# Kernel tuning notes

Measured on AMD Instinct MI355X. Metric: run time of the kernel, lower is better.

The kernel has to match this reference:

```python
import jax, jax.numpy as jnp
import numpy as np

BN_EPS = 1e-5


def setup_inputs() -> dict:
    key = jax.random.key(0)
    ks = jax.random.split(key, 12)
    N, E, H, INV = 100000, 500000, 128, 16
    DIN = 2 * H + INV  # 272
    x_send = jax.random.normal(ks[0], (N, H), dtype=jnp.float32)
    x_rec = jax.random.normal(ks[1], (N, H), dtype=jnp.float32)
    index = jax.random.randint(ks[2], (2, E), 0, N, dtype=jnp.int64)
    edge_attr = jax.random.normal(ks[3], (E, INV), dtype=jnp.float32)
    # message_mlp = BatchNorm1d(272) -> Linear(272,128) -> SiLU  (eval-mode BN)
    bn_gamma = jax.random.normal(ks[4], (DIN,), dtype=jnp.float32) * 0.1 + 1.0
    bn_beta = jax.random.normal(ks[5], (DIN,), dtype=jnp.float32) * 0.1
    bn_mean = jax.random.normal(ks[6], (DIN,), dtype=jnp.float32) * 0.1
    bn_var = jax.random.uniform(ks[7], (DIN,), dtype=jnp.float32) + 0.5
    W1 = jax.random.normal(ks[8], (DIN, H), dtype=jnp.float32) / np.sqrt(DIN)
    b1 = jnp.zeros((H,), dtype=jnp.float32)
    # edge_inf_mlp = Linear(128,1) -> Sigmoid
    W2 = jax.random.normal(ks[9], (H, 1), dtype=jnp.float32) / np.sqrt(H)
    b2 = jnp.zeros((1,), dtype=jnp.float32)
    return {"x_send": x_send, "x_rec": x_rec, "index": index, "edge_attr": edge_attr,
            "bn_gamma": bn_gamma, "bn_beta": bn_beta, "bn_mean": bn_mean, "bn_var": bn_var,
            "W1": W1, "b1": b1, "W2": W2, "b2": b2}


def reference(x_send, x_rec, index, edge_attr, bn_gamma, bn_beta, bn_mean, bn_var, W1, b1, W2, b2):
    idx_send, idx_rec = index[0], index[1]
    # gather + concat -> [E, 2H + INV]
    state = jnp.concatenate((x_send[idx_send], x_rec[idx_rec], edge_attr), axis=1)
    # eval-mode BatchNorm1d
    state = (state - bn_mean) * (bn_gamma * jax.lax.rsqrt(bn_var + BN_EPS)) + bn_beta
    # Linear + SiLU
    messages = jax.nn.silu(state @ W1 + b1)  # [E, H]
    # edge gating: Linear(H,1) + Sigmoid
    edge_weights = jax.nn.sigmoid(messages @ W2 + b2)  # [E, 1]
    # scatter_add aggregation over receiving nodes
    return jax.ops.segment_sum(messages * edge_weights, idx_rec, num_segments=x_rec.shape[0])
```

## Files before the change

kernel.cpp:

```cpp
#include <hip/hip_runtime.h>
#include <hip/hip_bf16.h>
#include <hip/hip_fp16.h>
#include <math.h>

#define HDIM 128
#define INVD 16
#define DIN 272
#define NKT 9

typedef __attribute__((ext_vector_type(4))) float f32x4;
typedef __attribute__((ext_vector_type(8))) short bf16x8;
typedef __attribute__((ext_vector_type(2))) __fp16 fp16x2;

__device__ inline short f2bf(float f) {
    union { float f; unsigned u; } v; v.f = f;
    unsigned r = v.u + 0x7FFFu + ((v.u >> 16) & 1u);
    return (short)(r >> 16);
}

__device__ inline unsigned cvt_pk_bf16(float a, float b) {
    unsigned r;
    asm("v_cvt_pk_bf16_f32 %0, %1, %2" : "=v"(r) : "v"(a), "v"(b));
    return r;
}

template<int MODE>
__global__ __launch_bounds__(256, 2) void etnn_kernel(
    const float* __restrict__ x_send,
    const float* __restrict__ x_rec,
    const int*   __restrict__ index,
    const float* __restrict__ edge_attr,
    const float* __restrict__ bn_gamma,
    const float* __restrict__ bn_beta,
    const float* __restrict__ bn_mean,
    const float* __restrict__ bn_var,
    const float* __restrict__ W1,
    const float* __restrict__ b1,
    const float* __restrict__ W2,
    const float* __restrict__ b2,
    float* __restrict__ out,
    __half* __restrict__ ws,
    int E, int nIter)
{
    __shared__ short btab[NKT * 8 * 64 * 8];
    __shared__ float scl[DIN];
    __shared__ float shf[DIN];
    __shared__ float bias2[2][HDIM];
    __shared__ float biasT[HDIM];

    const int tid = threadIdx.x;
    const int l  = tid & 63;
    const int lr = l & 15;
    const int lg = l >> 4;

    for (int c = tid; c < DIN; c += 256) {
        float sc = bn_gamma[c] * rsqrtf(bn_var[c] + 1e-5f);
        scl[c] = sc;
        shf[c] = bn_beta[c] - bn_mean[c] * sc;
    }
    __syncthreads();

    for (int f = tid; f < NKT * 8 * 64; f += 256) {
        const int kk  = f >> 9;
        const int cb  = (f >> 6) & 7;
        const int ln  = f & 63;
        const int k0  = kk * 32 + (ln >> 4) * 8;
        const int col = cb * 16 + (ln & 15);
        bf16x8 bv;
        #pragma unroll
        for (int j = 0; j < 8; ++j) {
            const int k = k0 + j;
            float v = (k < DIN) ? scl[k] * W1[k * HDIM + col] : 0.f;
            bv[j] = f2bf(v);
        }
        *(bf16x8*)&btab[f * 8] = bv;
    }
    {
        const int col  = tid & 127;
        const int half = tid >> 7;
        float s = 0.f;
        for (int k = half * 136; k < half * 136 + 136; ++k)
            s += shf[k] * W1[k * HDIM + col];
        bias2[half][col] = s;
    }
    __syncthreads();
    if (tid < HDIM) biasT[tid] = b1[tid] + bias2[0][tid] + bias2[1][tid];
    __syncthreads();

    float biasv[8], w2v[8];
    #pragma unroll
    for (int cb = 0; cb < 8; ++cb) {
        biasv[cb] = biasT[cb * 16 + lr];
        w2v[cb]   = W2[cb * 16 + lr];
    }
    const float b2v = b2[0];
    const bool evn = !(lr & 1);

    auto issueGather = [&](int pc, int is, int ir,
                           f32x4* Ls, f32x4* Lr, f32x4* La) {
        const f32x4* ps = (const f32x4*)(x_send + (size_t)is * HDIM);
        const f32x4* pr = (const f32x4*)(x_rec  + (size_t)ir * HDIM);
        #pragma unroll
        for (int kk = 0; kk < 4; ++kk) {
            Ls[kk * 2]     = ps[kk * 8 + lg * 2];
            Ls[kk * 2 + 1] = ps[kk * 8 + lg * 2 + 1];
            Lr[kk * 2]     = pr[kk * 8 + lg * 2];
            Lr[kk * 2 + 1] = pr[kk * 8 + lg * 2 + 1];
        }
        if (lg < 2) {
            const f32x4* pa = (const f32x4*)(edge_attr + (size_t)pc * INVD + lg * 8);
            La[0] = pa[0]; La[1] = pa[1];
        } else {
            La[0] = (f32x4){0.f, 0.f, 0.f, 0.f};
            La[1] = (f32x4){0.f, 0.f, 0.f, 0.f};
        }
    };

    auto computeTile = [&](int e0, int ir,
                           f32x4* Ls, f32x4* Lr, f32x4* La) {
        f32x4 acc[8];
        #pragma unroll
        for (int cb = 0; cb < 8; ++cb) acc[cb] = (f32x4){0.f, 0.f, 0.f, 0.f};

        #pragma unroll
        for (int kk = 0; kk < NKT; ++kk) {
            f32x4 lo = (kk < 4) ? Ls[kk * 2]     : (kk < 8) ? Lr[(kk - 4) * 2]     : La[0];
            f32x4 hi = (kk < 4) ? Ls[kk * 2 + 1] : (kk < 8) ? Lr[(kk - 4) * 2 + 1] : La[1];
            union { bf16x8 v; unsigned u[4]; } a;
            a.u[0] = cvt_pk_bf16(lo[0], lo[1]);
            a.u[1] = cvt_pk_bf16(lo[2], lo[3]);
            a.u[2] = cvt_pk_bf16(hi[0], hi[1]);
            a.u[3] = cvt_pk_bf16(hi[2], hi[3]);
            #pragma unroll
            for (int cb = 0; cb < 8; ++cb) {
                bf16x8 b = *(const bf16x8*)&btab[((kk * 8 + cb) * 64 + l) * 8];
                acc[cb] = __builtin_amdgcn_mfma_f32_16x16x32_bf16(a.v, b, acc[cb], 0, 0, 0);
            }
        }

        float p[4] = {0.f, 0.f, 0.f, 0.f};
        #pragma unroll
        for (int cb = 0; cb < 8; ++cb) {
            #pragma unroll
            for (int q = 0; q < 4; ++q) {
                float z = acc[cb][q] + biasv[cb];
                float m = z / (1.f + __expf(-z));
                acc[cb][q] = m;
                p[q] += m * w2v[cb];
            }
        }
        #pragma unroll
        for (int q = 0; q < 4; ++q) {
            p[q] += __shfl_xor(p[q], 1, 64);
            p[q] += __shfl_xor(p[q], 2, 64);
            p[q] += __shfl_xor(p[q], 4, 64);
            p[q] += __shfl_xor(p[q], 8, 64);
        }

        #pragma unroll
        for (int q = 0; q < 4; ++q) {
            const int row = lg * 4 + q;
            if (e0 + row < E) {
                const int irq = __shfl(ir, row, 64);
                const float g = 1.f / (1.f + __expf(-(p[q] + b2v)));
                if constexpr (MODE == 1) {
                    float m[8];
                    #pragma unroll
                    for (int cb = 0; cb < 8; ++cb) m[cb] = acc[cb][q] * g;
                    #pragma unroll
                    for (int c = 0; c < 4; ++c) {
                        float x0 = __shfl_xor(m[2 * c],     1, 64);
                        float x1 = __shfl_xor(m[2 * c + 1], 1, 64);
                        float va = evn ? m[2 * c] : x1;
                        float vb = evn ? x0       : m[2 * c + 1];
                        union { fp16x2 h; unsigned u; } pk;
                        pk.h = __builtin_amdgcn_cvt_pkrtz(va, vb);
                        const int col0 = evn ? (32 * c + lr) : (32 * c + 15 + lr);
                        unsigned long long a =
                            (unsigned long long)(ws + (size_t)irq * HDIM + col0);
                        asm volatile("global_atomic_pk_add_f16 %0, %1, off"
                                     :: "v"(a), "v"(pk.u) : "memory");
                    }
                } else {
                    float* orow = out + (size_t)irq * HDIM + lr;
                    #pragma unroll
                    for (int cb = 0; cb < 8; ++cb)
                        atomicAdd(orow + cb * 16, acc[cb][q] * g);
                }
            }
        }
    };

    const int gw = blockIdx.x * 4 + (tid >> 6);
    const int NW = gridDim.x * 4;

    for (int it = gw; it < nIter; it += 2 * NW) {
        const int itB  = it + NW;
        const bool hasB = itB < nIter;

        const int posA = it * 16 + lr;
        const int pcA  = (posA < E) ? posA : E - 1;
        const int isA  = index[pcA];
        const int irA  = index[E + pcA];

        int pcB = 0, isB = 0, irB = 0;
        if (hasB) {
            const int posB = itB * 16 + lr;
            pcB = (posB < E) ? posB : E - 1;
            isB = index[pcB];
            irB = index[E + pcB];
        }

        f32x4 LsA[8], LrA[8], LaA[2];
        f32x4 LsB[8], LrB[8], LaB[2];
        issueGather(pcA, isA, irA, LsA, LrA, LaA);
        if (hasB) issueGather(pcB, isB, irB, LsB, LrB, LaB);

        computeTile(it * 16, irA, LsA, LrA, LaA);
        if (hasB) computeTile(itB * 16, irB, LsB, LrB, LaB);
    }
}

__global__ __launch_bounds__(256) void cvt_kernel(const __half* __restrict__ ws,
                                                  float* __restrict__ out, int n) {
    int i = (blockIdx.x * 256 + threadIdx.x) * 4;
    if (i < n) {
        const __half2* p = (const __half2*)(ws + i);
        float2 a = __half22float2(p[0]);
        float2 b = __half22float2(p[1]);
        f32x4 v = {a.x, a.y, b.x, b.y};
        *(f32x4*)(out + i) = v;
    }
}

extern "C" void kernel_launch(void* const* d_in, const int* in_sizes, int n_in,
                              void* d_out, int out_size, void* d_ws, size_t ws_size,
                              hipStream_t stream) {
    const float* x_send    = (const float*)d_in[0];
    const float* x_rec     = (const float*)d_in[1];
    const int*   index     = (const int*)d_in[2];
    const float* edge_attr = (const float*)d_in[3];
    const float* bn_gamma  = (const float*)d_in[4];
    const float* bn_beta   = (const float*)d_in[5];
    const float* bn_mean   = (const float*)d_in[6];
    const float* bn_var    = (const float*)d_in[7];
    const float* W1        = (const float*)d_in[8];
    const float* b1        = (const float*)d_in[9];
    const float* W2        = (const float*)d_in[10];
    const float* b2        = (const float*)d_in[11];
    float* out = (float*)d_out;

    const int E = in_sizes[3] / INVD;
    const int N = in_sizes[0] / HDIM;
    const int nIter = (E + 15) / 16;
    const int grid = 512;

    const size_t accBytes = (size_t)N * HDIM * sizeof(__half);
    if (ws_size >= accBytes) {
        __half* ws = (__half*)d_ws;
        hipMemsetAsync(ws, 0, accBytes, stream);
        etnn_kernel<1><<<grid, 256, 0, stream>>>(x_send, x_rec, index, edge_attr,
                                                 bn_gamma, bn_beta, bn_mean, bn_var,
                                                 W1, b1, W2, b2, out, ws, E, nIter);
        const int n = N * HDIM;
        cvt_kernel<<<(n / 4 + 255) / 256, 256, 0, stream>>>(ws, out, n);
    } else {
        hipMemsetAsync(d_out, 0, (size_t)out_size * sizeof(float), stream);
        etnn_kernel<0><<<grid, 256, 0, stream>>>(x_send, x_rec, index, edge_attr,
                                                 bn_gamma, bn_beta, bn_mean, bn_var,
                                                 W1, b1, W2, b2, out, nullptr, E, nIter);
    }
}
```

Before: 221.3 us.

## Software-pipeline gathers across iterations and use hardware reciprocal in activations

Restructures the per-wave loop into a rotating double-buffer. The next tile's gathers and the index loads two tiles ahead are issued before the current tile is computed, with scheduling barriers to keep that ordering. It also replaces the divisions in SiLU and sigmoid with a raw v_rcp_f32 instruction. The goal is to hide gather latency behind MFMA work and cut the cost of division, at the price of more live registers and slightly lower reciprocal precision.

```diff
diff --git a/kernel.cpp b/kernel.cpp
--- a/kernel.cpp
+++ b/kernel.cpp
@@ -21,6 +21,12 @@
 __device__ inline unsigned cvt_pk_bf16(float a, float b) {
     unsigned r;
     asm("v_cvt_pk_bf16_f32 %0, %1, %2" : "=v"(r) : "v"(a), "v"(b));
+    return r;
+}
+
+__device__ inline float fast_rcp(float x) {
+    float r;
+    asm("v_rcp_f32 %0, %1" : "=v"(r) : "v"(x));
     return r;
 }
 
@@ -96,6 +102,17 @@
     const float b2v = b2[0];
     const bool evn = !(lr & 1);
 
+    const int gw = blockIdx.x * 4 + (tid >> 6);
+    const int NW = gridDim.x * 4;
+
+    auto ldIdx = [&](int itx, int& pc, int& is, int& ir) {
+        int pos = itx * 16 + lr;
+        pc = (pos < E) ? pos : E - 1;
+        if (pc < 0) pc = 0;
+        is = index[pc];
+        ir = index[E + pc];
+    };
+
     auto issueGather = [&](int pc, int is, int ir,
                            f32x4* Ls, f32x4* Lr, f32x4* La) {
         const f32x4* ps = (const f32x4*)(x_send + (size_t)is * HDIM);
@@ -144,7 +161,7 @@
             #pragma unroll
             for (int q = 0; q < 4; ++q) {
                 float z = acc[cb][q] + biasv[cb];
-                float m = z / (1.f + __expf(-z));
+                float m = z * fast_rcp(1.f + __expf(-z));
                 acc[cb][q] = m;
                 p[q] += m * w2v[cb];
             }
@@ -162,7 +179,7 @@
             const int row = lg * 4 + q;
             if (e0 + row < E) {
                 const int irq = __shfl(ir, row, 64);
-                const float g = 1.f / (1.f + __expf(-(p[q] + b2v)));
+                const float g = fast_rcp(1.f + __expf(-(p[q] + b2v)));
                 if constexpr (MODE == 1) {
                     float m[8];
                     #pragma unroll
@@ -191,33 +208,33 @@
         }
     };
 
-    const int gw = blockIdx.x * 4 + (tid >> 6);
-    const int NW = gridDim.x * 4;
+    f32x4 LsA[8], LrA[8], LaA[2];
+    f32x4 LsB[8], LrB[8], LaB[2];
+
+    if (gw >= nIter) return;
+
+    int pc0, is0, ir0;
+    int pc1, is1, ir1;
+    ldIdx(gw, pc0, is0, ir0);
+    issueGather(pc0, is0, ir0, LsA, LrA, LaA);
+    ldIdx(gw + NW, pc1, is1, ir1);
 
     for (int it = gw; it < nIter; it += 2 * NW) {
-        const int itB  = it + NW;
-        const bool hasB = itB < nIter;
-
-        const int posA = it * 16 + lr;
-        const int pcA  = (posA < E) ? posA : E - 1;
-        const int isA  = index[pcA];
-        const int irA  = index[E + pcA];
-
-        int pcB = 0, isB = 0, irB = 0;
-        if (hasB) {
-            const int posB = itB * 16 + lr;
-            pcB = (posB < E) ? posB : E - 1;
-            isB = index[pcB];
-            irB = index[E + pcB];
-        }
-
-        f32x4 LsA[8], LrA[8], LaA[2];
-        f32x4 LsB[8], LrB[8], LaB[2];
-        issueGather(pcA, isA, irA, LsA, LrA, LaA);
-        if (hasB) issueGather(pcB, isB, irB, LsB, LrB, LaB);
-
-        computeTile(it * 16, irA, LsA, LrA, LaA);
-        if (hasB) computeTile(itB * 16, irB, LsB, LrB, LaB);
+        issueGather(pc1, is1, ir1, LsB, LrB, LaB);
+        int pc2, is2, ir2;
+        ldIdx(it + 2 * NW, pc2, is2, ir2);
+        __builtin_amdgcn_sched_barrier(0);
+        computeTile(it * 16, ir0, LsA, LrA, LaA);
+
+        issueGather(pc2, is2, ir2, LsA, LrA, LaA);
+        int pc3, is3, ir3;
+        ldIdx(it + 3 * NW, pc3, is3, ir3);
+        __builtin_amdgcn_sched_barrier(0);
+        if (it + NW < nIter)
+            computeTile((it + NW) * 16, ir1, LsB, LrB, LaB);
+
+        pc0 = pc2; is0 = is2; ir0 = ir2;
+        pc1 = pc3; is1 = is3; ir1 = ir3;
     }
 }
 
```

Result: faster. 198.6 us (-10.3%).

## Trade two-tile software pipelining for 512-thread blocks and fast reciprocal

Applied to the files above, without the earlier changes.

Drops the per-warp double-tile gather/compute pipelining and runs one 16-edge tile per iteration, which cuts register pressure. Blocks grow to 512 threads with a launch bound of 4 blocks per CU, so more waves are resident and gather latency is hidden by occupancy instead of in-thread prefetch. The precomputed LDS B table is shared by twice as many waves. The divides in SiLU and sigmoid become raw v_rcp_f32, trading a little accuracy for fewer instructions. The risk is that a 512x4 bound may force register spills or lower real occupancy given the ~74KB LDS table per block.

```diff
diff --git a/kernel.cpp b/kernel.cpp
--- a/kernel.cpp
+++ b/kernel.cpp
@@ -24,8 +24,14 @@
     return r;
 }
 
+__device__ inline float fast_rcp(float x) {
+    float r;
+    asm("v_rcp_f32 %0, %1" : "=v"(r) : "v"(x));
+    return r;
+}
+
 template<int MODE>
-__global__ __launch_bounds__(256, 2) void etnn_kernel(
+__global__ __launch_bounds__(512, 4) void etnn_kernel(
     const float* __restrict__ x_send,
     const float* __restrict__ x_rec,
     const int*   __restrict__ index,
@@ -53,14 +59,14 @@
     const int lr = l & 15;
     const int lg = l >> 4;
 
-    for (int c = tid; c < DIN; c += 256) {
+    for (int c = tid; c < DIN; c += 512) {
         float sc = bn_gamma[c] * rsqrtf(bn_var[c] + 1e-5f);
         scl[c] = sc;
         shf[c] = bn_beta[c] - bn_mean[c] * sc;
     }
     __syncthreads();
 
-    for (int f = tid; f < NKT * 8 * 64; f += 256) {
+    for (int f = tid; f < NKT * 8 * 64; f += 512) {
         const int kk  = f >> 9;
         const int cb  = (f >> 6) & 7;
         const int ln  = f & 63;
@@ -75,7 +81,7 @@
         }
         *(bf16x8*)&btab[f * 8] = bv;
     }
-    {
+    if (tid < 256) {
         const int col  = tid & 127;
         const int half = tid >> 7;
         float s = 0.f;
@@ -96,10 +102,19 @@
     const float b2v = b2[0];
     const bool evn = !(lr & 1);
 
-    auto issueGather = [&](int pc, int is, int ir,
-                           f32x4* Ls, f32x4* Lr, f32x4* La) {
+    const int gw = blockIdx.x * 8 + (tid >> 6);
+    const int NW = gridDim.x * 8;
+
+    for (int it = gw; it < nIter; it += NW) {
+        const int e0 = it * 16;
+        const int pos = e0 + lr;
+        const int pc  = (pos < E) ? pos : E - 1;
+        const int is = index[pc];
+        const int ir = index[E + pc];
+
         const f32x4* ps = (const f32x4*)(x_send + (size_t)is * HDIM);
         const f32x4* pr = (const f32x4*)(x_rec  + (size_t)ir * HDIM);
+        f32x4 Ls[8], Lr[8], La[2];
         #pragma unroll
         for (int kk = 0; kk < 4; ++kk) {
             Ls[kk * 2]     = ps[kk * 8 + lg * 2];
@@ -114,10 +129,7 @@
             La[0] = (f32x4){0.f, 0.f, 0.f, 0.f};
             La[1] = (f32x4){0.f, 0.f, 0.f, 0.f};
         }
-    };
-
-    auto computeTile = [&](int e0, int ir,
-                           f32x4* Ls, f32x4* Lr, f32x4* La) {
+
         f32x4 acc[8];
         #pragma unroll
         for (int cb = 0; cb < 8; ++cb) acc[cb] = (f32x4){0.f, 0.f, 0.f, 0.f};
@@ -144,7 +156,7 @@
             #pragma unroll
             for (int q = 0; q < 4; ++q) {
                 float z = acc[cb][q] + biasv[cb];
-                float m = z / (1.f + __expf(-z));
+                float m = z * fast_rcp(1.f + __expf(-z));
                 acc[cb][q] = m;
                 p[q] += m * w2v[cb];
             }
@@ -162,7 +174,7 @@
             const int row = lg * 4 + q;
             if (e0 + row < E) {
                 const int irq = __shfl(ir, row, 64);
-                const float g = 1.f / (1.f + __expf(-(p[q] + b2v)));
+                const float g = fast_rcp(1.f + __expf(-(p[q] + b2v)));
                 if constexpr (MODE == 1) {
                     float m[8];
                     #pragma unroll
@@ -189,35 +201,6 @@
                 }
             }
         }
-    };
-
-    const int gw = blockIdx.x * 4 + (tid >> 6);
-    const int NW = gridDim.x * 4;
-
-    for (int it = gw; it < nIter; it += 2 * NW) {
-        const int itB  = it + NW;
-        const bool hasB = itB < nIter;
-
-        const int posA = it * 16 + lr;
-        const int pcA  = (posA < E) ? posA : E - 1;
-        const int isA  = index[pcA];
-        const int irA  = index[E + pcA];
-
-        int pcB = 0, isB = 0, irB = 0;
-        if (hasB) {
-            const int posB = itB * 16 + lr;
-            pcB = (posB < E) ? posB : E - 1;
-            isB = index[pcB];
-            irB = index[E + pcB];
-        }
-
-        f32x4 LsA[8], LrA[8], LaA[2];
-        f32x4 LsB[8], LrB[8], LaB[2];
-        issueGather(pcA, isA, irA, LsA, LrA, LaA);
-        if (hasB) issueGather(pcB, isB, irB, LsB, LrB, LaB);
-
-        computeTile(it * 16, irA, LsA, LrA, LaA);
-        if (hasB) computeTile(itB * 16, irB, LsB, LrB, LaB);
     }
 }
 
@@ -259,14 +242,14 @@
     if (ws_size >= accBytes) {
         __half* ws = (__half*)d_ws;
         hipMemsetAsync(ws, 0, accBytes, stream);
-        etnn_kernel<1><<<grid, 256, 0, stream>>>(x_send, x_rec, index, edge_attr,
+        etnn_kernel<1><<<grid, 512, 0, stream>>>(x_send, x_rec, index, edge_attr,
                                                  bn_gamma, bn_beta, bn_mean, bn_var,
                                                  W1, b1, W2, b2, out, ws, E, nIter);
         const int n = N * HDIM;
         cvt_kernel<<<(n / 4 + 255) / 256, 256, 0, stream>>>(ws, out, n);
     } else {
         hipMemsetAsync(d_out, 0, (size_t)out_size * sizeof(float), stream);
-        etnn_kernel<0><<<grid, 256, 0, stream>>>(x_send, x_rec, index, edge_attr,
+        etnn_kernel<0><<<grid, 512, 0, stream>>>(x_send, x_rec, index, edge_attr,
                                                  bn_gamma, bn_beta, bn_mean, bn_var,
                                                  W1, b1, W2, b2, out, nullptr, E, nIter);
     }
```

After: 211.0 us. -4.6%, faster.
